# Optimization experiments

Hardware: AMD Instinct MI355X
Metric: run time of the kernel (lower is better)

The kernel has to match this reference:

```python
import jax, jax.numpy as jnp
import numpy as np

E, DEPTH, H, T_BLOCK, VOC = 1024, 8, 16, 2048, 256
DH = E // H
B, T = 4, 2048
EPS = 1e-5


def _layernorm(x, g, b):
    mu = jnp.mean(x, axis=-1, keepdims=True)
    var = jnp.mean(jnp.square(x - mu), axis=-1, keepdims=True)
    return (x - mu) * jax.lax.rsqrt(var + EPS) * g + b


def setup_inputs() -> dict:
    key = jax.random.key(0)
    ks = iter(jax.random.split(key, 32))

    def xav(k, shape):
        fan_in, fan_out = shape[-2], shape[-1]
        lim = np.sqrt(6.0 / (fan_in + fan_out))
        return jax.random.uniform(k, shape, jnp.float32, -lim, lim)

    inp = {
        "tokens": jax.random.randint(next(ks), (B, T), 0, VOC),
        "emb_w": xav(next(ks), (VOC, E)),
        "pos_w": xav(next(ks), (T_BLOCK, E)),
        # per-layer stacked params
        "Wq": xav(next(ks), (DEPTH, H, E, DH)),
        "Wk": xav(next(ks), (DEPTH, H, E, DH)),
        "Wv": xav(next(ks), (DEPTH, H, E, DH)),
        "Wo": xav(next(ks), (DEPTH, E, E)),        # stored [in, out]
        "ln1_g": jnp.ones((DEPTH, E)), "ln1_b": jnp.zeros((DEPTH, E)),
        "W1": xav(next(ks), (DEPTH, E, 4 * E)), "b1": jnp.zeros((DEPTH, 4 * E)),
        "W2": xav(next(ks), (DEPTH, 4 * E, E)), "b2": jnp.zeros((DEPTH, E)),
        "ln2_g": jnp.ones((DEPTH, E)), "ln2_b": jnp.zeros((DEPTH, E)),
        "lnf_g": jnp.ones((E,)), "lnf_b": jnp.zeros((E,)),
        "Wu": xav(next(ks), (E, 2)), "bu": jnp.zeros((2,)),
    }
    return inp


def _forward(tokens, emb_w, pos_w, Wq, Wk, Wv, Wo, ln1_g, ln1_b,
             W1, b1, W2, b2, ln2_g, ln2_b, lnf_g, lnf_b, Wu, bu):
    Tlen = tokens.shape[1]
    x = emb_w[tokens] + pos_w[:Tlen]                       # [B, T, E]
    scale = 1.0 / jnp.sqrt(jnp.float32(Tlen))              # NOTE: original divides by sqrt(seq_len)
    for l in range(Wq.shape[0]):
        h = _layernorm(x, ln1_g[l], ln1_b[l])
        q = jnp.einsum('hed,bte->bhtd', Wq[l], h)
        k = jnp.einsum('hed,bte->bhtd', Wk[l], h)
        v = jnp.einsum('hed,bte->bhtd', Wv[l], h)
        scores = jnp.einsum('bhtd,bhsd->bhts', q, k) * scale
        attn = jax.nn.softmax(scores, axis=-1)
        att = jnp.einsum('bhts,bhsd->bhtd', attn, v)       # [B, H, T, DH]
        att = att.transpose(0, 2, 1, 3).reshape(x.shape)   # b t (h d)
        x = x + att @ Wo[l]
        h = _layernorm(x, ln2_g[l], ln2_b[l])
        x = x + jax.nn.relu(h @ W1[l] + b1[l]) @ W2[l] + b2[l]
    x = _layernorm(x, lnf_g, lnf_b)
    return x @ Wu + bu                                     # [B, T, 2]


def reference(tokens, emb_w, pos_w, Wq, Wk, Wv, Wo, ln1_g, ln1_b,
              W1, b1, W2, b2, ln2_g, ln2_b, lnf_g, lnf_b, Wu, bu):
    return _forward(tokens, emb_w, pos_w, Wq, Wk, Wv, Wo, ln1_g, ln1_b,
                    W1, b1, W2, b2, ln2_g, ln2_b, lnf_g, lnf_b, Wu, bu)
```

## Files before the change

### kernel.cpp

```cpp
#include <hip/hip_runtime.h>
#include <hip/hip_bf16.h>
#include <math.h>

#define E_DIM 1024
#define T_SEQ 2048
#define NH 16
#define DHEAD 64
#define NB 4
#define NLAYER 8

typedef __attribute__((ext_vector_type(8))) short bf16x8;
typedef __attribute__((ext_vector_type(4))) short short4v;
typedef __attribute__((ext_vector_type(4))) float f32x4;

#if __has_builtin(__builtin_amdgcn_exp2f)
#define EXP2(x) __builtin_amdgcn_exp2f(x)
#else
#define EXP2(x) exp2f(x)
#endif

static __device__ __forceinline__ short f2bf(float f) {
  union { __hip_bfloat16 h; short s; } u;
  u.h = __float2bfloat16(f);
  return u.s;
}
static __device__ __forceinline__ float bf2f(short s) {
  union { unsigned u; float f; } v;
  v.u = ((unsigned)(unsigned short)s) << 16;
  return v.f;
}

static __device__ __forceinline__ int xcd_swz(int orig, int nwg) {
  return (orig & 7) * (nwg >> 3) + (orig >> 3);
}

__global__ __launch_bounds__(256) void embed_kernel(const int* __restrict__ tokens,
    const float* __restrict__ emb, const float* __restrict__ pos, float* __restrict__ x) {
  int idx = blockIdx.x * 256 + threadIdx.x;
  int bt = idx >> 10;
  int e  = idx & 1023;
  int t  = bt & (T_SEQ - 1);
  int tok = tokens[bt];
  x[idx] = emb[tok * E_DIM + e] + pos[t * E_DIM + e];
}

__global__ __launch_bounds__(256) void ln_bf16_kernel(const float* __restrict__ x,
    const float* __restrict__ g, const float* __restrict__ b, short* __restrict__ out) {
  __shared__ float s1[4], s2[4];
  int row = blockIdx.x;
  const float4* xr = (const float4*)(x + (size_t)row * E_DIM);
  float4 xv = xr[threadIdx.x];
  float s = xv.x + xv.y + xv.z + xv.w;
  float q = xv.x*xv.x + xv.y*xv.y + xv.z*xv.z + xv.w*xv.w;
  #pragma unroll
  for (int off = 32; off; off >>= 1) {
    s += __shfl_xor(s, off, 64);
    q += __shfl_xor(q, off, 64);
  }
  int lane = threadIdx.x & 63, wid = threadIdx.x >> 6;
  if (lane == 0) { s1[wid] = s; s2[wid] = q; }
  __syncthreads();
  float mean = (s1[0] + s1[1] + s1[2] + s1[3]) * (1.0f / E_DIM);
  float ms   = (s2[0] + s2[1] + s2[2] + s2[3]) * (1.0f / E_DIM);
  float rstd = rsqrtf(ms - mean * mean + 1e-5f);
  float4 gv = ((const float4*)g)[threadIdx.x];
  float4 bv = ((const float4*)b)[threadIdx.x];
  short4v ov;
  ov.x = f2bf((xv.x - mean) * rstd * gv.x + bv.x);
  ov.y = f2bf((xv.y - mean) * rstd * gv.y + bv.y);
  ov.z = f2bf((xv.z - mean) * rstd * gv.z + bv.z);
  ov.w = f2bf((xv.w - mean) * rstd * gv.w + bv.w);
  *(short4v*)(out + (size_t)row * E_DIM + threadIdx.x * 4) = ov;
}

struct PrepP {
  const float *s0, *s1, *s2, *s3, *s4, *s5;
  short *d0, *d1, *d2, *d3, *d4, *d5;
};

__global__ void prep_kernel(PrepP p) {
  __shared__ float tile[32][33];
  int bid = blockIdx.x;
  const float* src; short* dst; int K, N, kb, local;
  if (bid < 1024)      { src = p.s0; dst = p.d0; K = 1024; N = 64;   kb = 32;  local = bid; }
  else if (bid < 2048) { src = p.s1; dst = p.d1; K = 1024; N = 64;   kb = 32;  local = bid - 1024; }
  else if (bid < 3072) { src = p.s2; dst = p.d2; K = 1024; N = 64;   kb = 32;  local = bid - 2048; }
  else if (bid < 4096) { src = p.s3; dst = p.d3; K = 1024; N = 1024; kb = 32;  local = bid - 3072; }
  else if (bid < 8192) { src = p.s4; dst = p.d4; K = 1024; N = 4096; kb = 32;  local = bid - 4096; }
  else                 { src = p.s5; dst = p.d5; K = 4096; N = 1024; kb = 128; local = bid - 8192; }
  int per = kb * (N >> 5);
  int z = local / per, rem = local % per;
  int k0 = (rem % kb) * 32, n0 = (rem / kb) * 32;
  src += (size_t)z * K * N;
  dst += (size_t)z * N * K;
  int tx = threadIdx.x, ty = threadIdx.y;
  #pragma unroll
  for (int i = 0; i < 4; ++i)
    tile[ty + 8 * i][tx] = src[(size_t)(k0 + ty + 8 * i) * N + n0 + tx];
  __syncthreads();
  #pragma unroll
  for (int i = 0; i < 4; ++i)
    dst[(size_t)(n0 + ty + 8 * i) * K + k0 + tx] = f2bf(tile[tx][ty + 8 * i]);
}

struct GemmP {
  const short* A; const short* B; void* C;
  const float* bias; const float* res;
  long sAb, sAt, sAh;
  long sBh, sBd;
  long sCb, sCt, sCh;
  int K; float alpha; int alphaN; int gridx;
  int relu; int cbf16; int hasbias; int hasres;
};

__global__ __launch_bounds__(256) void gemm_bf16(GemmP p) {
  __shared__ __align__(16) short As[128 * 64];
  __shared__ __align__(16) short Bs[128 * 64];
  const int t = threadIdx.x;
  const int lane = t & 63, wid = t >> 6;
  const int wr = wid >> 1, wc = wid & 1;
  const int wg = xcd_swz(blockIdx.x, gridDim.x);
  const long bm = (long)(wg / p.gridx) * 128, bn = (long)(wg % p.gridx) * 128;

  const int prow = t >> 3;
  const int pcol = t & 7;
  long aRow[4], bRow[4];
  int wIdx[4];
  #pragma unroll
  for (int c = 0; c < 4; ++c) {
    int r = c * 32 + prow;
    long gm = bm + r, gn = bn + r;
    aRow[c] = (gm >> 11) * p.sAb + (gm & 2047) * p.sAt;
    bRow[c] = (gn >> 6) * p.sBh + (gn & 63) * p.sBd;
    wIdx[c] = r * 64 + ((pcol ^ (r & 7)) << 3);
  }

  const int rA = lane & 15;
  const int g  = lane >> 4;
  int aOff[4][2], bOff[4][2];
  #pragma unroll
  for (int f = 0; f < 4; ++f) {
    int rowa = wr * 64 + f * 16 + rA;
    int rowb = wc * 64 + f * 16 + rA;
    #pragma unroll
    for (int kk = 0; kk < 2; ++kk) {
      aOff[f][kk] = rowa * 64 + (((g + kk * 4) ^ (rowa & 7)) << 3);
      bOff[f][kk] = rowb * 64 + (((g + kk * 4) ^ (rowb & 7)) << 3);
    }
  }

  f32x4 acc[4][4] = {};
  bf16x8 ra[4], rb[4];
  {
    long kc = (long)(pcol * 8);
    long ka = (kc >> 6) * p.sAh + (kc & 63);
    #pragma unroll
    for (int c = 0; c < 4; ++c) {
      ra[c] = *(const bf16x8*)(p.A + aRow[c] + ka);
      rb[c] = *(const bf16x8*)(p.B + bRow[c] + kc);
    }
  }

  for (int k0 = 0; k0 < p.K; k0 += 64) {
    __syncthreads();
    #pragma unroll
    for (int c = 0; c < 4; ++c) {
      *(bf16x8*)&As[wIdx[c]] = ra[c];
      *(bf16x8*)&Bs[wIdx[c]] = rb[c];
    }
    __syncthreads();
    if (k0 + 64 < p.K) {
      long kc = (long)(k0 + 64 + pcol * 8);
      long ka = (kc >> 6) * p.sAh + (kc & 63);
      #pragma unroll
      for (int c = 0; c < 4; ++c) {
        ra[c] = *(const bf16x8*)(p.A + aRow[c] + ka);
        rb[c] = *(const bf16x8*)(p.B + bRow[c] + kc);
      }
    }
    #pragma unroll
    for (int kk = 0; kk < 2; ++kk) {
      bf16x8 af[4], bf[4];
      #pragma unroll
      for (int f = 0; f < 4; ++f) {
        af[f] = *(const bf16x8*)&As[aOff[f][kk]];
        bf[f] = *(const bf16x8*)&Bs[bOff[f][kk]];
      }
      #pragma unroll
      for (int i = 0; i < 4; ++i)
        #pragma unroll
        for (int j = 0; j < 4; ++j)
          acc[i][j] = __builtin_amdgcn_mfma_f32_16x16x32_bf16(af[i], bf[j], acc[i][j], 0, 0, 0);
    }
  }

  float bias4[4], aa4[4];
  long ncol[4];
  #pragma unroll
  for (int j = 0; j < 4; ++j) {
    long n = bn + wc * 64 + j * 16 + rA;
    ncol[j] = (n >> 6) * p.sCh + (n & 63);
    bias4[j] = p.hasbias ? p.bias[n] : 0.f;
    aa4[j] = (n < p.alphaN) ? p.alpha : 1.0f;
  }
  #pragma unroll
  for (int i = 0; i < 4; ++i) {
    #pragma unroll
    for (int r = 0; r < 4; ++r) {
      long m = bm + wr * 64 + i * 16 + g * 4 + r;
      long mb = (m >> 11) * p.sCb + (m & 2047) * p.sCt;
      #pragma unroll
      for (int j = 0; j < 4; ++j) {
        long ca = mb + ncol[j];
        float v = aa4[j] * acc[i][j][r] + bias4[j];
        if (p.relu) v = fmaxf(v, 0.f);
        if (p.hasres) v += p.res[ca];
        if (p.cbf16) ((short*)p.C)[ca] = f2bf(v);
        else ((float*)p.C)[ca] = v;
      }
    }
  }
}

__global__ __launch_bounds__(512) void attn_mfma_kernel(const short* __restrict__ qkv,
                                                        short* __restrict__ att) {
  __shared__ __align__(16) short Ks[64 * 64];
  __shared__ __align__(16) short Vt[64 * 64];
  __shared__ __align__(16) short Pq[8 * 16 * 64];

  const int t = threadIdx.x;
  const int lane = t & 63, wid = t >> 6;
  const int wg = xcd_swz(blockIdx.x, gridDim.x);
  const int bh = wg >> 4;
  const int b = bh >> 4, h = bh & 15;
  const int q0blk = (wg & 15) * 128;
  const int rA = lane & 15;
  const int g  = lane >> 4;
  const int xq = (rA & 7) << 3;
  const float L2E = 1.4426950408889634f;

  const short* Qg = qkv + (size_t)b * 6291456 + (size_t)h * 131072;
  const short* Kg = Qg + 2097152;
  const short* Vg = Qg + 4194304;

  const int q0w = q0blk + wid * 16;
  bf16x8 qf0 = *(const bf16x8*)(Qg + (size_t)(q0w + rA) * DHEAD + g * 8);
  bf16x8 qf1 = *(const bf16x8*)(Qg + (size_t)(q0w + rA) * DHEAD + 32 + g * 8);

  short* Pw = Pq + wid * 1024;
  const int ss = t >> 3, sp = t & 7;

  float mrun = -1e30f, lrun = 0.f;
  f32x4 acco[4] = {};

  bf16x8 kreg = *(const bf16x8*)(Kg + (size_t)ss * DHEAD + sp * 8);
  bf16x8 vreg = *(const bf16x8*)(Vg + (size_t)ss * DHEAD + sp * 8);

  for (int tile = 0; tile < T_SEQ / 64; ++tile) {
    __syncthreads();
    *(bf16x8*)&Ks[ss * 64 + ((sp ^ (ss & 7)) << 3)] = kreg;
    #pragma unroll
    for (int j = 0; j < 8; ++j) {
      int d = sp * 8 + j;
      Vt[d * 64 + ((ss + 8 * (sp + j)) & 63)] = vreg[j];
    }
    __syncthreads();
    if (tile + 1 < T_SEQ / 64) {
      kreg = *(const bf16x8*)(Kg + (size_t)((tile + 1) * 64 + ss) * DHEAD + sp * 8);
      vreg = *(const bf16x8*)(Vg + (size_t)((tile + 1) * 64 + ss) * DHEAD + sp * 8);
    }

    f32x4 accs[4];
    __builtin_amdgcn_s_setprio(1);
    #pragma unroll
    for (int st = 0; st < 4; ++st) {
      int srow = st * 16 + rA;
      bf16x8 kf0 = *(const bf16x8*)&Ks[srow * 64 + ((g ^ (rA & 7)) << 3)];
      bf16x8 kf1 = *(const bf16x8*)&Ks[srow * 64 + (((g + 4) ^ (rA & 7)) << 3)];
      f32x4 z = {};
      z = __builtin_amdgcn_mfma_f32_16x16x32_bf16(kf0, qf0, z, 0, 0, 0);
      accs[st] = __builtin_amdgcn_mfma_f32_16x16x32_bf16(kf1, qf1, z, 0, 0, 0);
    }
    __builtin_amdgcn_s_setprio(0);

    float tm = accs[0][0];
    #pragma unroll
    for (int st = 0; st < 4; ++st)
      #pragma unroll
      for (int r = 0; r < 4; ++r) tm = fmaxf(tm, accs[st][r]);
    tm = fmaxf(tm, __shfl_xor(tm, 16));
    tm = fmaxf(tm, __shfl_xor(tm, 32));

    float pv[16];
    if (__all(tm - mrun <= 8.0f)) {
      float mL = mrun * L2E;
      float ts = 0.f;
      #pragma unroll
      for (int st = 0; st < 4; ++st)
        #pragma unroll
        for (int r = 0; r < 4; ++r) {
          float e = EXP2(fmaf(accs[st][r], L2E, -mL));
          pv[st * 4 + r] = e;
          ts += e;
        }
      lrun += ts;
    } else {
      float mnew = fmaxf(mrun, tm);
      float mL = mnew * L2E;
      float corr = EXP2((mrun - mnew) * L2E);
      float ts = 0.f;
      #pragma unroll
      for (int st = 0; st < 4; ++st)
        #pragma unroll
        for (int r = 0; r < 4; ++r) {
          float e = EXP2(fmaf(accs[st][r], L2E, -mL));
          pv[st * 4 + r] = e;
          ts += e;
        }
      lrun = lrun * corr + ts;
      mrun = mnew;
      float c4r[4];
      #pragma unroll
      for (int r = 0; r < 4; ++r) c4r[r] = __shfl(corr, g * 4 + r);
      #pragma unroll
      for (int dt = 0; dt < 4; ++dt)
        #pragma unroll
        for (int r = 0; r < 4; ++r) acco[dt][r] *= c4r[r];
    }

    #pragma unroll
    for (int st = 0; st < 4; ++st) {
      short4v pk;
      pk.x = f2bf(pv[st * 4 + 0]);
      pk.y = f2bf(pv[st * 4 + 1]);
      pk.z = f2bf(pv[st * 4 + 2]);
      pk.w = f2bf(pv[st * 4 + 3]);
      *(short4v*)&Pw[(rA * 64 + st * 16 + g * 4) ^ xq] = pk;
    }
    asm volatile("s_waitcnt lgkmcnt(0)" ::: "memory");

    __builtin_amdgcn_s_setprio(1);
    #pragma unroll
    for (int sk = 0; sk < 2; ++sk) {
      bf16x8 pf = *(const bf16x8*)&Pw[(rA * 64 + sk * 32 + g * 8) ^ xq];
      #pragma unroll
      for (int dt = 0; dt < 4; ++dt) {
        int d = dt * 16 + rA;
        bf16x8 vf = *(const bf16x8*)&Vt[d * 64 +
            ((sk * 32 + g * 8 + 8 * (dt * 2 + (rA >> 3) + (rA & 7))) & 63)];
        acco[dt] = __builtin_amdgcn_mfma_f32_16x16x32_bf16(pf, vf, acco[dt], 0, 0, 0);
      }
    }
    __builtin_amdgcn_s_setprio(0);
  }

  lrun += __shfl_xor(lrun, 16);
  lrun += __shfl_xor(lrun, 32);
  float l4[4];
  #pragma unroll
  for (int r = 0; r < 4; ++r) l4[r] = 1.0f / __shfl(lrun, g * 4 + r);
  #pragma unroll
  for (int dt = 0; dt < 4; ++dt)
    #pragma unroll
    for (int r = 0; r < 4; ++r)
      att[(size_t)bh * T_SEQ * DHEAD + (size_t)(q0w + g * 4 + r) * DHEAD + dt * 16 + rA] =
          f2bf(acco[dt][r] * l4[r]);
}

__global__ __launch_bounds__(256) void head_kernel(const short* __restrict__ h,
    const float* __restrict__ Wu, const float* __restrict__ bu, float* __restrict__ out) {
  __shared__ float sm[8];
  int row = blockIdx.x;
  const short* hr = h + (size_t)row * E_DIM;
  float a0 = 0.f, a1 = 0.f;
  for (int i = threadIdx.x; i < E_DIM; i += 256) {
    float hv = bf2f(hr[i]);
    a0 = fmaf(hv, Wu[i * 2 + 0], a0);
    a1 = fmaf(hv, Wu[i * 2 + 1], a1);
  }
  #pragma unroll
  for (int off = 32; off; off >>= 1) {
    a0 += __shfl_xor(a0, off, 64);
    a1 += __shfl_xor(a1, off, 64);
  }
  int lane = threadIdx.x & 63, wid = threadIdx.x >> 6;
  if (lane == 0) { sm[wid] = a0; sm[4 + wid] = a1; }
  __syncthreads();
  if (threadIdx.x == 0) {
    out[row * 2 + 0] = sm[0] + sm[1] + sm[2] + sm[3] + bu[0];
    out[row * 2 + 1] = sm[4] + sm[5] + sm[6] + sm[7] + bu[1];
  }
}

static inline void launch_gemm(hipStream_t stream, int N,
    const short* A, long sAb, long sAt, long sAh,
    const short* B, long sBh, long sBd,
    void* C, long sCb, long sCt, long sCh,
    const float* bias, const float* res, int K, float alpha, int alphaN,
    int relu, int cbf16) {
  GemmP p;
  p.A = A; p.B = B; p.C = C; p.bias = bias; p.res = res;
  p.sAb = sAb; p.sAt = sAt; p.sAh = sAh;
  p.sBh = sBh; p.sBd = sBd;
  p.sCb = sCb; p.sCt = sCt; p.sCh = sCh;
  p.K = K; p.alpha = alpha; p.alphaN = alphaN; p.gridx = N / 128;
  p.relu = relu; p.cbf16 = cbf16;
  p.hasbias = bias != nullptr; p.hasres = res != nullptr;
  int nwg = (N / 128) * ((NB * T_SEQ) / 128);
  gemm_bf16<<<nwg, 256, 0, stream>>>(p);
}

extern "C" void kernel_launch(void* const* d_in, const int* in_sizes, int n_in,
                              void* d_out, int out_size, void* d_ws, size_t ws_size,
                              hipStream_t stream) {
  const int*   tokens = (const int*)d_in[0];
  const float* emb_w  = (const float*)d_in[1];
  const float* pos_w  = (const float*)d_in[2];
  const float* Wq     = (const float*)d_in[3];
  const float* Wk     = (const float*)d_in[4];
  const float* Wv     = (const float*)d_in[5];
  const float* Wo     = (const float*)d_in[6];
  const float* ln1_g  = (const float*)d_in[7];
  const float* ln1_b  = (const float*)d_in[8];
  const float* W1     = (const float*)d_in[9];
  const float* b1     = (const float*)d_in[10];
  const float* W2     = (const float*)d_in[11];
  const float* b2     = (const float*)d_in[12];
  const float* ln2_g  = (const float*)d_in[13];
  const float* ln2_b  = (const float*)d_in[14];
  const float* lnf_g  = (const float*)d_in[15];
  const float* lnf_b  = (const float*)d_in[16];
  const float* Wu     = (const float*)d_in[17];
  const float* bu     = (const float*)d_in[18];
  float* out = (float*)d_out;

  char* ws = (char*)d_ws;
  float* X     = (float*)(ws);
  short* Hb    = (short*)(ws + 33554432);
  short* QKVb  = (short*)(ws + 50331648);
  short* FFH   = (short*)(ws + 100663296);
  short* WqkvT = (short*)(ws + 167772160);
  short* WoT   = (short*)(ws + 174063616);
  short* W1T   = (short*)(ws + 176160768);
  short* W2T   = (short*)(ws + 184549376);

  const float scale = 0.022097086912079608f;

  embed_kernel<<<32768, 256, 0, stream>>>(tokens, emb_w, pos_w, X);

  for (int l = 0; l < NLAYER; ++l) {
    PrepP pp;
    pp.s0 = Wq + (size_t)l * 1048576; pp.d0 = WqkvT;
    pp.s1 = Wk + (size_t)l * 1048576; pp.d1 = WqkvT + 1048576;
    pp.s2 = Wv + (size_t)l * 1048576; pp.d2 = WqkvT + 2097152;
    pp.s3 = Wo + (size_t)l * 1048576; pp.d3 = WoT;
    pp.s4 = W1 + (size_t)l * 4194304; pp.d4 = W1T;
    pp.s5 = W2 + (size_t)l * 4194304; pp.d5 = W2T;
    prep_kernel<<<12288, dim3(32, 8), 0, stream>>>(pp);

    ln_bf16_kernel<<<8192, 256, 0, stream>>>(X, ln1_g + l * 1024, ln1_b + l * 1024, Hb);

    launch_gemm(stream, 3072, Hb, 2097152, 1024, 64, WqkvT, 65536, 1024,
                QKVb, 6291456, 64, 131072, nullptr, nullptr, 1024, scale, 1024, 0, 1);

    attn_mfma_kernel<<<1024, 512, 0, stream>>>(QKVb, Hb);

    launch_gemm(stream, 1024, Hb, 2097152, 64, 131072, WoT, 65536, 1024,
                X, 2097152, 1024, 64, nullptr, X, 1024, 1.0f, 0, 0, 0);

    ln_bf16_kernel<<<8192, 256, 0, stream>>>(X, ln2_g + l * 1024, ln2_b + l * 1024, Hb);

    launch_gemm(stream, 4096, Hb, 2097152, 1024, 64, W1T, 65536, 1024,
                FFH, 8388608, 4096, 64, b1 + (size_t)l * 4096, nullptr, 1024, 1.0f, 0, 1, 1);
    launch_gemm(stream, 1024, FFH, 8388608, 4096, 64, W2T, 262144, 4096,
                X, 2097152, 1024, 64, b2 + (size_t)l * 1024, X, 4096, 1.0f, 0, 0, 0);
  }

  ln_bf16_kernel<<<8192, 256, 0, stream>>>(X, lnf_g, lnf_b, Hb);
  head_kernel<<<8192, 256, 0, stream>>>(Hb, Wu, bu, out);
}
```

Before: 3.442 ms.

## Load GEMM tiles directly into LDS with global_load_lds, dropping register prefetch

Replaces the register-staged prefetch of A/B tiles in the bf16 GEMM with direct global-to-LDS 16-byte loads, and removes the XOR swizzle from the LDS layout. This saves VGPRs and the register-to-LDS store instructions. In exchange it loses the overlap of the next tile's global load with the current MFMA work, since loads now sit between two barriers. The unswizzled layout may also cause LDS bank conflicts on fragment reads. A dependency on the sAh stride being a per-64-K step is also assumed.

```diff
diff --git a/kernel.cpp b/kernel.cpp
--- a/kernel.cpp
+++ b/kernel.cpp
@@ -28,6 +28,12 @@
   union { unsigned u; float f; } v;
   v.u = ((unsigned)(unsigned short)s) << 16;
   return v.f;
+}
+
+static __device__ __forceinline__ void gload16(const short* g, short* l) {
+  __builtin_amdgcn_global_load_lds(
+      (const __attribute__((address_space(1))) unsigned*)(g),
+      (__attribute__((address_space(3))) unsigned*)(l), 16, 0, 0);
 }
 
 static __device__ __forceinline__ int xcd_swz(int orig, int nwg) {
@@ -122,17 +128,17 @@
   const int wg = xcd_swz(blockIdx.x, gridDim.x);
   const long bm = (long)(wg / p.gridx) * 128, bn = (long)(wg % p.gridx) * 128;
 
-  const int prow = t >> 3;
-  const int pcol = t & 7;
-  long aRow[4], bRow[4];
-  int wIdx[4];
+  const short* aSrc[4]; const short* bSrc[4];
+  short* aDst[4]; short* bDst[4];
   #pragma unroll
   for (int c = 0; c < 4; ++c) {
-    int r = c * 32 + prow;
-    long gm = bm + r, gn = bn + r;
-    aRow[c] = (gm >> 11) * p.sAb + (gm & 2047) * p.sAt;
-    bRow[c] = (gn >> 6) * p.sBh + (gn & 63) * p.sBd;
-    wIdx[c] = r * 64 + ((pcol ^ (r & 7)) << 3);
+    int sidx = wid * 256 + c * 64 + lane;
+    int row = sidx >> 3, chunk = sidx & 7;
+    long gm = bm + row, gn = bn + row;
+    aSrc[c] = p.A + (gm >> 11) * p.sAb + (gm & 2047) * p.sAt + chunk * 8;
+    bSrc[c] = p.B + (gn >> 6) * p.sBh + (gn & 63) * p.sBd + chunk * 8;
+    aDst[c] = As + wid * 2048 + c * 512;
+    bDst[c] = Bs + wid * 2048 + c * 512;
   }
 
   const int rA = lane & 15;
@@ -140,44 +146,24 @@
   int aOff[4][2], bOff[4][2];
   #pragma unroll
   for (int f = 0; f < 4; ++f) {
-    int rowa = wr * 64 + f * 16 + rA;
-    int rowb = wc * 64 + f * 16 + rA;
     #pragma unroll
     for (int kk = 0; kk < 2; ++kk) {
-      aOff[f][kk] = rowa * 64 + (((g + kk * 4) ^ (rowa & 7)) << 3);
-      bOff[f][kk] = rowb * 64 + (((g + kk * 4) ^ (rowb & 7)) << 3);
+      aOff[f][kk] = (wr * 64 + f * 16 + rA) * 64 + (g + kk * 4) * 8;
+      bOff[f][kk] = (wc * 64 + f * 16 + rA) * 64 + (g + kk * 4) * 8;
     }
   }
 
   f32x4 acc[4][4] = {};
-  bf16x8 ra[4], rb[4];
-  {
-    long kc = (long)(pcol * 8);
-    long ka = (kc >> 6) * p.sAh + (kc & 63);
-    #pragma unroll
-    for (int c = 0; c < 4; ++c) {
-      ra[c] = *(const bf16x8*)(p.A + aRow[c] + ka);
-      rb[c] = *(const bf16x8*)(p.B + bRow[c] + kc);
-    }
-  }
 
   for (int k0 = 0; k0 < p.K; k0 += 64) {
     __syncthreads();
     #pragma unroll
-    for (int c = 0; c < 4; ++c) {
-      *(bf16x8*)&As[wIdx[c]] = ra[c];
-      *(bf16x8*)&Bs[wIdx[c]] = rb[c];
-    }
+    for (int c = 0; c < 4; ++c) gload16(aSrc[c], aDst[c]);
+    #pragma unroll
+    for (int c = 0; c < 4; ++c) gload16(bSrc[c], bDst[c]);
     __syncthreads();
-    if (k0 + 64 < p.K) {
-      long kc = (long)(k0 + 64 + pcol * 8);
-      long ka = (kc >> 6) * p.sAh + (kc & 63);
-      #pragma unroll
-      for (int c = 0; c < 4; ++c) {
-        ra[c] = *(const bf16x8*)(p.A + aRow[c] + ka);
-        rb[c] = *(const bf16x8*)(p.B + bRow[c] + kc);
-      }
-    }
+    #pragma unroll
+    for (int c = 0; c < 4; ++c) { aSrc[c] += p.sAh; bSrc[c] += 64; }
     #pragma unroll
     for (int kk = 0; kk < 2; ++kk) {
       bf16x8 af[4], bf[4];
```

After: 4.055 ms. +17.8%, slower.
